# Performance work log

Measured on AMD Instinct MI355X. Metric: run time of the kernel, lower is better.

Reference implementation:

```python
import jax, jax.numpy as jnp
import numpy as np

DEPTH = 11          # tree depth
D = 1024            # input_width
H = 32              # hidden_width (leaf MLP)
O = 1024            # output_width
B = 4096            # flattened token batch
N_LEAVES = 2 ** DEPTH
N_NODES = 2 ** DEPTH - 1


def setup_inputs() -> dict:
    key = jax.random.key(0)
    ks = jax.random.split(key, 7)
    f1 = 1.0 / np.sqrt(D)
    f2 = 1.0 / np.sqrt(H)
    u = lambda k, shape, f: jax.random.uniform(k, shape, jnp.float32, -f, f)
    return {
        "x": jax.random.normal(ks[0], (B, D), jnp.float32),
        "node_weights": u(ks[1], (N_NODES, D), f1),
        "node_biases": u(ks[2], (N_NODES,), f1),   # (n_nodes,1) in torch; flattened
        "w1s": u(ks[3], (N_LEAVES, D, H), f1),
        "b1s": u(ks[4], (N_LEAVES, H), f1),
        "w2s": u(ks[5], (N_LEAVES, H, O), f2),
        "b2s": u(ks[6], (N_LEAVES, O), f2),
    }


def reference(x, node_weights, node_biases, w1s, b1s, w2s, b2s):
    # --- hard tree descent (eval_forward) ---
    nodes = jnp.zeros((x.shape[0],), jnp.int32)
    for i in range(DEPTH):  # fixed small loop over tree depth
        w = node_weights[nodes]                       # [B, D] gathered plane coeffs
        b = node_biases[nodes]                        # [B]
        score = jnp.einsum('bd,bd->b', x, w) + b      # per-sample dot product
        choice = (score >= 0).astype(jnp.int32)
        platform = 2 ** i - 1
        next_platform = 2 ** (i + 1) - 1
        nodes = (nodes - platform) * 2 + choice + next_platform
    leaves = nodes - (2 ** DEPTH - 1)                 # [B] leaf index per sample

    # --- per-sample leaf MLP with gathered weights ---
    h = jax.nn.relu(jnp.einsum('bd,bdh->bh', x, w1s[leaves]) + b1s[leaves])  # [B, H]
    out = jnp.einsum('bh,bho->bo', h, w2s[leaves]) + b2s[leaves]             # [B, O]
    return out
```

## Files before the change

kernel.cpp:

```cpp
#include <hip/hip_runtime.h>

#define DEPTH 11
#define D 1024
#define H 32
#define OW 1024
#define B 4096
#define N_LEAVES 2048
#define N_NODES 2047
#define SMAX 4
#define MAX_ITEMS 3072
#define NBLK 768
#define MAXK 4

typedef float f32x4 __attribute__((ext_vector_type(4)));
typedef __attribute__((address_space(3))) void lds_void;
typedef const __attribute__((address_space(1))) void glb_void;

#define SB __builtin_amdgcn_sched_barrier(0)
#define WAITV(N) do { asm volatile("s_waitcnt vmcnt(" #N ")" ::: "memory"); SB; } while (0)
#define WAITLG0  do { asm volatile("s_waitcnt lgkmcnt(0)" ::: "memory"); SB; } while (0)
#define BARRIER  do { WAITLG0; __builtin_amdgcn_s_barrier(); \
                      asm volatile("" ::: "memory"); SB; } while (0)
#define GLOAD(dst, ptr) \
    asm volatile("global_load_dwordx4 %0, %1, off" : "=&v"(dst) : "v"(ptr) : "memory")

__global__ __launch_bounds__(256) void descent_kernel(
    const float* __restrict__ x, const float* __restrict__ nw,
    const float* __restrict__ nb, int* __restrict__ leaf,
    int* __restrict__ rnk, int* __restrict__ count)
{
    int lane = threadIdx.x & 63;
    int wv   = threadIdx.x >> 6;
    int samp = blockIdx.x * 4 + wv;

    const float4* xp = (const float4*)(x + (size_t)samp * D);
    float4 xf[4];
#pragma unroll
    for (int k = 0; k < 4; k++) xf[k] = xp[lane + 64 * k];

    int node = 0;
#pragma unroll
    for (int i = 0; i < DEPTH; i++) {
        const float4* wp = (const float4*)(nw + (size_t)node * D);
        double s = 0.0;
#pragma unroll
        for (int k = 0; k < 4; k++) {
            float4 wf = wp[lane + 64 * k];
            s += (double)xf[k].x * (double)wf.x;
            s += (double)xf[k].y * (double)wf.y;
            s += (double)xf[k].z * (double)wf.z;
            s += (double)xf[k].w * (double)wf.w;
        }
#pragma unroll
        for (int m = 32; m >= 1; m >>= 1) s += __shfl_xor(s, m, 64);
        double score = s + (double)nb[node];
        int choice = (score >= 0.0) ? 1 : 0;
        node = 2 * node + 1 + choice;
    }
    int lf = node - N_NODES;
    if (lane == 0) {
        leaf[samp] = lf;
        rnk[samp]  = atomicAdd(&count[lf], 1);
    }
}

__global__ __launch_bounds__(256) void scan_kernel(
    const int* __restrict__ count, int* __restrict__ offsets)
{
    __shared__ int tot[256];
    int t = threadIdx.x;
    int c[8], s = 0;
#pragma unroll
    for (int k = 0; k < 8; k++) { c[k] = count[t * 8 + k]; s += c[k]; }
    tot[t] = s;
    __syncthreads();
    for (int off = 1; off < 256; off <<= 1) {
        int v = (t >= off) ? tot[t - off] : 0;
        __syncthreads();
        tot[t] += v;
        __syncthreads();
    }
    int base = (t > 0) ? tot[t - 1] : 0;
#pragma unroll
    for (int k = 0; k < 8; k++) { offsets[t * 8 + k] = base; base += c[k]; }
}

__global__ __launch_bounds__(256) void scatter_kernel(
    const int* __restrict__ leaf, const int* __restrict__ rnk,
    const int* __restrict__ offsets, int* __restrict__ bucket)
{
    int i = blockIdx.x * 256 + threadIdx.x;
    bucket[offsets[leaf[i]] + rnk[i]] = i;
}

__global__ __launch_bounds__(256) void build_items_kernel(
    const int* __restrict__ count, int* __restrict__ items,
    int* __restrict__ nitems)
{
    int l = blockIdx.x * 256 + threadIdx.x;
    int c = count[l];
    if (c > 0) {
        int k = (c + SMAX - 1) / SMAX;
        int base = atomicAdd(nitems, k);
        for (int i = 0; i < k; i++)
            items[base + i] = l | ((i * SMAX) << 11);
    }
}

__global__ __launch_bounds__(256, 3) void mlp_kernel(
    const float* __restrict__ x, const float* __restrict__ w1s,
    const float* __restrict__ b1s, const float* __restrict__ w2s,
    const float* __restrict__ b2s, const int* __restrict__ offsets,
    const int* __restrict__ count, const int* __restrict__ bucket,
    const int* __restrict__ items, const int* __restrict__ nitems,
    float* __restrict__ out)
{
    __shared__ __align__(16) float xs[SMAX][D];
    __shared__ __align__(16) float pl1[4][SMAX][32];
    __shared__ __align__(16) float hs[SMAX][32];
    __shared__ __align__(16) float b1l[2][4][64];
    __shared__ __align__(16) float b2l[2][4][256];
    __shared__ int md_leaf[MAXK];
    __shared__ int md_sid[MAXK][4];

    const int tid = threadIdx.x, lane = tid & 63, wave = tid >> 6;
    const int dg = lane >> 3, lane4 = lane * 4;
    const int bid = blockIdx.x;

    int nit = nitems[0];
    if (tid < MAXK) {
        int idx = bid + tid * NBLK;
        if (idx < nit) {
            int it = items[idx];
            int l = it & (N_LEAVES - 1), st = it >> 11;
            int c = count[l] - st;
            int S = (c < SMAX) ? c : SMAX;
            int off = offsets[l] + st;
            md_leaf[tid] = l;
            for (int s = 0; s < 4; s++)
                md_sid[tid][s] = bucket[off + ((s < S) ? s : (S - 1))];
        }
    }
    __syncthreads();
    if (bid >= nit) return;
    int n_my = (nit - bid + NBLK - 1) / NBLK;
    if (n_my > MAXK) n_my = MAXK;

    f32x4 w1r[2][4];
    f32x4 w2r[16];

#define L1I(base, cc, bb) do { _Pragma("unroll") \
    for (int u = 0; u < 4; u++) \
        GLOAD(w1r[bb][u], (base) + (cc) * 1024 + u * 256 + lane4); } while (0)

#define L1C(cc, bb) do { _Pragma("unroll") \
    for (int u = 0; u < 4; u++) { \
        f32x4 wv_ = w1r[bb][u]; \
        _Pragma("unroll") \
        for (int s = 0; s < 4; s++) \
            acc[s] += xs[s][wave * 256 + (cc) * 32 + u * 8 + dg] * wv_; } } while (0)

    int lc = md_leaf[0];
    const float* w1x = w1s + (size_t)lc * 32768 + wave * 8192;
    {
#pragma unroll
        for (int pp = 0; pp < 4; pp++)
            __builtin_amdgcn_global_load_lds(
                (glb_void*)(x + (size_t)md_sid[0][pp] * D + wave * 256 + lane4),
                (lds_void*)(&xs[pp][wave * 256]), 16, 0, 0);
        __builtin_amdgcn_global_load_lds(
            (glb_void*)(b1s + lc * H + ((lane < 32) ? lane : 31)),
            (lds_void*)(&b1l[0][wave][0]), 4, 0, 0);
        __builtin_amdgcn_global_load_lds(
            (glb_void*)(b2s + (size_t)lc * OW + wave * 256 + lane4),
            (lds_void*)(&b2l[0][wave][0]), 16, 0, 0);
        L1I(w1x, 0, 0); L1I(w1x, 1, 1);
        L1I(w1x, 0, 0); L1I(w1x, 1, 1);
    }

    for (int k = 0; k < n_my; k++) {
        const int p  = k & 1, pn = p ^ 1;
        const int kn = (k + 1 < n_my) ? k + 1 : k;
        const int ln = md_leaf[kn];
        const float* w2x = w2s + (size_t)lc * 32768 + wave * 256;
        const float* w1n = w1s + (size_t)ln * 32768 + wave * 8192;
        int sidc[4];
#pragma unroll
        for (int s = 0; s < 4; s++) sidc[s] = md_sid[k][s];

        f32x4 acc[4] = {};

        WAITV(8); L1C(0, 0); L1I(w1x, 2, 0);
        WAITV(8); L1C(1, 1); L1I(w1x, 3, 1);
        WAITV(4); L1C(2, 0); L1I(w1x, 4, 0);
        WAITV(4); L1C(3, 1); L1I(w1x, 5, 1);
        WAITV(4); L1C(4, 0); L1I(w1x, 6, 0);
        WAITV(4); L1C(5, 1); L1I(w1x, 7, 1);
        WAITV(4); L1C(6, 0);
#pragma unroll
        for (int j = 0; j < 8; j++) GLOAD(w2r[j], w2x + j * 1024 + lane4);
        WAITV(8); L1C(7, 1);
#pragma unroll
        for (int j = 8; j < 16; j++) GLOAD(w2r[j], w2x + j * 1024 + lane4);

#pragma unroll
        for (int m = 8; m <= 32; m <<= 1)
#pragma unroll
            for (int s = 0; s < 4; s++)
#pragma unroll
                for (int e = 0; e < 4; e++)
                    acc[s][e] += __shfl_xor(acc[s][e], m, 64);
        if (dg == 0) {
#pragma unroll
            for (int s = 0; s < 4; s++)
                *(f32x4*)&pl1[wave][s][(lane & 7) * 4] = acc[s];
        }
        BARRIER;
        if (tid < 128) {
            int s2 = tid >> 5, j2 = tid & 31;
            float sum = pl1[0][s2][j2] + pl1[1][s2][j2] + pl1[2][s2][j2] +
                        pl1[3][s2][j2] + b1l[p][tid >> 6][j2];
            hs[s2][j2] = fmaxf(sum, 0.f);
        }
        BARRIER;

        f32x4 o[4] = {};
#pragma unroll
        for (int jj = 0; jj < 32; jj++) {
            if (jj == 31) { WAITV(14); } else { WAITV(15); }
            f32x4 w = w2r[jj & 15];
#pragma unroll
            for (int s = 0; s < 4; s++) o[s] += hs[s][jj] * w;
            if (jj < 16) {
                GLOAD(w2r[jj & 15], w2x + (jj + 16) * 1024 + lane4);
            } else if (jj < 20) {
                const int pp = jj - 16;
                __builtin_amdgcn_global_load_lds(
                    (glb_void*)(x + (size_t)md_sid[kn][pp] * D + wave * 256 + lane4),
                    (lds_void*)(&xs[pp][wave * 256]), 16, 0, 0);
            } else if (jj == 20) {
                __builtin_amdgcn_global_load_lds(
                    (glb_void*)(b1s + ln * H + ((lane < 32) ? lane : 31)),
                    (lds_void*)(&b1l[pn][wave][0]), 4, 0, 0);
            } else if (jj == 21) {
                __builtin_amdgcn_global_load_lds(
                    (glb_void*)(b2s + (size_t)ln * OW + wave * 256 + lane4),
                    (lds_void*)(&b2l[pn][wave][0]), 16, 0, 0);
            } else if (jj < 26) {
                GLOAD(w1r[0][jj - 22], w1n + (jj - 22) * 256 + lane4);
            } else if (jj < 30) {
                GLOAD(w1r[1][jj - 26], w1n + 1024 + (jj - 26) * 256 + lane4);
            }
        }

        f32x4 bv = *(const f32x4*)&b2l[p][wave][lane4];
#pragma unroll
        for (int s = 0; s < 4; s++) {
            f32x4 ov = o[s] + bv;
            *(f32x4*)(out + (size_t)sidc[s] * OW + wave * 256 + lane4) = ov;
        }
        lc = ln;
        w1x = w1n;
    }
#undef L1I
#undef L1C
}

extern "C" void kernel_launch(void* const* d_in, const int* in_sizes, int n_in,
                              void* d_out, int out_size, void* d_ws, size_t ws_size,
                              hipStream_t stream)
{
    const float* x   = (const float*)d_in[0];
    const float* nw  = (const float*)d_in[1];
    const float* nb  = (const float*)d_in[2];
    const float* w1s = (const float*)d_in[3];
    const float* b1s = (const float*)d_in[4];
    const float* w2s = (const float*)d_in[5];
    const float* b2s = (const float*)d_in[6];
    float* out = (float*)d_out;

    int* leaf    = (int*)d_ws;
    int* rnk     = leaf + B;
    int* count   = rnk + B;
    int* offsets = count + N_LEAVES;
    int* bucket  = offsets + N_LEAVES;
    int* items   = bucket + B;
    int* nitems  = items + MAX_ITEMS;

    hipMemsetAsync(count, 0, N_LEAVES * sizeof(int), stream);
    hipMemsetAsync(nitems, 0, sizeof(int), stream);
    descent_kernel<<<B / 4, 256, 0, stream>>>(x, nw, nb, leaf, rnk, count);
    scan_kernel<<<1, 256, 0, stream>>>(count, offsets);
    scatter_kernel<<<B / 256, 256, 0, stream>>>(leaf, rnk, offsets, bucket);
    build_items_kernel<<<N_LEAVES / 256, 256, 0, stream>>>(count, items, nitems);
    mlp_kernel<<<NBLK, 256, 0, stream>>>(x, w1s, b1s, w2s, b2s,
                                         offsets, count, bucket,
                                         items, nitems, out);
}
```

Measured before the change: 128.1 us.

## Fuse item building into scan, drop a barrier, and hand-schedule the layer-2 loop

```diff
diff --git a/kernel.cpp b/kernel.cpp
--- a/kernel.cpp
+++ b/kernel.cpp
@@ -64,11 +64,14 @@
     }
 }
 
-__global__ __launch_bounds__(256) void scan_kernel(
-    const int* __restrict__ count, int* __restrict__ offsets)
+__global__ __launch_bounds__(256) void scanbuild_kernel(
+    const int* __restrict__ count, int* __restrict__ offsets,
+    int* __restrict__ items, int* __restrict__ nitems)
 {
     __shared__ int tot[256];
+    __shared__ int ln;
     int t = threadIdx.x;
+    if (t == 0) ln = 0;
     int c[8], s = 0;
 #pragma unroll
     for (int k = 0; k < 8; k++) { c[k] = count[t * 8 + k]; s += c[k]; }
@@ -81,8 +84,20 @@
         __syncthreads();
     }
     int base = (t > 0) ? tot[t - 1] : 0;
-#pragma unroll
-    for (int k = 0; k < 8; k++) { offsets[t * 8 + k] = base; base += c[k]; }
+    int myit = 0;
+#pragma unroll
+    for (int k = 0; k < 8; k++) myit += (c[k] + SMAX - 1) / SMAX;
+    int ibase = (myit > 0) ? atomicAdd(&ln, myit) : 0;
+#pragma unroll
+    for (int k = 0; k < 8; k++) {
+        offsets[t * 8 + k] = base;
+        int ki = (c[k] + SMAX - 1) / SMAX;
+        for (int i = 0; i < ki; i++)
+            items[ibase++] = (t * 8 + k) | ((i * SMAX) << 11);
+        base += c[k];
+    }
+    __syncthreads();
+    if (t == 0) nitems[0] = ln;
 }
 
 __global__ __launch_bounds__(256) void scatter_kernel(
@@ -91,20 +106,6 @@
 {
     int i = blockIdx.x * 256 + threadIdx.x;
     bucket[offsets[leaf[i]] + rnk[i]] = i;
-}
-
-__global__ __launch_bounds__(256) void build_items_kernel(
-    const int* __restrict__ count, int* __restrict__ items,
-    int* __restrict__ nitems)
-{
-    int l = blockIdx.x * 256 + threadIdx.x;
-    int c = count[l];
-    if (c > 0) {
-        int k = (c + SMAX - 1) / SMAX;
-        int base = atomicAdd(nitems, k);
-        for (int i = 0; i < k; i++)
-            items[base + i] = l | ((i * SMAX) << 11);
-    }
 }
 
 __global__ __launch_bounds__(256, 3) void mlp_kernel(
@@ -116,8 +117,8 @@
     float* __restrict__ out)
 {
     __shared__ __align__(16) float xs[SMAX][D];
-    __shared__ __align__(16) float pl1[4][SMAX][32];
-    __shared__ __align__(16) float hs[SMAX][32];
+    __shared__ __align__(16) float pl1[2][4][SMAX][32];
+    __shared__ __align__(16) float hs_w[4][SMAX][32];
     __shared__ __align__(16) float b1l[2][4][64];
     __shared__ __align__(16) float b2l[2][4][256];
     __shared__ int md_leaf[MAXK];
@@ -160,22 +161,26 @@
         for (int s = 0; s < 4; s++) \
             acc[s] += xs[s][wave * 256 + (cc) * 32 + u * 8 + dg] * wv_; } } while (0)
 
+#define STAGE_X(KK, PP) \
+    __builtin_amdgcn_global_load_lds( \
+        (glb_void*)(x + (size_t)md_sid[KK][PP] * D + wave * 256 + lane4), \
+        (lds_void*)(&xs[PP][wave * 256]), 16, 0, 0)
+#define STAGE_B1(LL, PP) \
+    __builtin_amdgcn_global_load_lds( \
+        (glb_void*)(b1s + (LL) * H + ((lane < 32) ? lane : 31)), \
+        (lds_void*)(&b1l[PP][wave][0]), 4, 0, 0)
+#define STAGE_B2(LL, PP) \
+    __builtin_amdgcn_global_load_lds( \
+        (glb_void*)(b2s + (size_t)(LL) * OW + wave * 256 + lane4), \
+        (lds_void*)(&b2l[PP][wave][0]), 16, 0, 0)
+
     int lc = md_leaf[0];
     const float* w1x = w1s + (size_t)lc * 32768 + wave * 8192;
     {
-#pragma unroll
-        for (int pp = 0; pp < 4; pp++)
-            __builtin_amdgcn_global_load_lds(
-                (glb_void*)(x + (size_t)md_sid[0][pp] * D + wave * 256 + lane4),
-                (lds_void*)(&xs[pp][wave * 256]), 16, 0, 0);
-        __builtin_amdgcn_global_load_lds(
-            (glb_void*)(b1s + lc * H + ((lane < 32) ? lane : 31)),
-            (lds_void*)(&b1l[0][wave][0]), 4, 0, 0);
-        __builtin_amdgcn_global_load_lds(
-            (glb_void*)(b2s + (size_t)lc * OW + wave * 256 + lane4),
-            (lds_void*)(&b2l[0][wave][0]), 16, 0, 0);
+        STAGE_X(0, 0); STAGE_X(0, 1); STAGE_X(0, 2); STAGE_X(0, 3);
+        STAGE_B1(lc, 0); STAGE_B2(lc, 0);
         L1I(w1x, 0, 0); L1I(w1x, 1, 1);
-        L1I(w1x, 0, 0); L1I(w1x, 1, 1);
+        L1I(w1x, 1, 1);
     }
 
     for (int k = 0; k < n_my; k++) {
@@ -190,16 +195,16 @@
 
         f32x4 acc[4] = {};
 
-        WAITV(8); L1C(0, 0); L1I(w1x, 2, 0);
-        WAITV(8); L1C(1, 1); L1I(w1x, 3, 1);
-        WAITV(4); L1C(2, 0); L1I(w1x, 4, 0);
-        WAITV(4); L1C(3, 1); L1I(w1x, 5, 1);
-        WAITV(4); L1C(4, 0); L1I(w1x, 6, 0);
-        WAITV(4); L1C(5, 1); L1I(w1x, 7, 1);
-        WAITV(4); L1C(6, 0);
+        WAITV(8); L1C(0, 0); SB; L1I(w1x, 2, 0);
+        WAITV(8); L1C(1, 1); SB; L1I(w1x, 3, 1);
+        WAITV(4); L1C(2, 0); SB; L1I(w1x, 4, 0);
+        WAITV(4); L1C(3, 1); SB; L1I(w1x, 5, 1);
+        WAITV(4); L1C(4, 0); SB; L1I(w1x, 6, 0);
+        WAITV(4); L1C(5, 1); SB; L1I(w1x, 7, 1);
+        WAITV(4); L1C(6, 0); SB;
 #pragma unroll
         for (int j = 0; j < 8; j++) GLOAD(w2r[j], w2x + j * 1024 + lane4);
-        WAITV(8); L1C(7, 1);
+        WAITV(8); L1C(7, 1); SB;
 #pragma unroll
         for (int j = 8; j < 16; j++) GLOAD(w2r[j], w2x + j * 1024 + lane4);
 
@@ -213,45 +218,63 @@
         if (dg == 0) {
 #pragma unroll
             for (int s = 0; s < 4; s++)
-                *(f32x4*)&pl1[wave][s][(lane & 7) * 4] = acc[s];
+                *(f32x4*)&pl1[p][wave][s][(lane & 7) * 4] = acc[s];
         }
         BARRIER;
-        if (tid < 128) {
-            int s2 = tid >> 5, j2 = tid & 31;
-            float sum = pl1[0][s2][j2] + pl1[1][s2][j2] + pl1[2][s2][j2] +
-                        pl1[3][s2][j2] + b1l[p][tid >> 6][j2];
-            hs[s2][j2] = fmaxf(sum, 0.f);
-        }
-        BARRIER;
-
+
+        {
+            int v = lane * 2, s2 = v >> 5, j2 = v & 31;
+            float ha = pl1[p][0][s2][j2] + pl1[p][1][s2][j2] +
+                       pl1[p][2][s2][j2] + pl1[p][3][s2][j2] + b1l[p][wave][j2];
+            float hb = pl1[p][0][s2][j2 + 1] + pl1[p][1][s2][j2 + 1] +
+                       pl1[p][2][s2][j2 + 1] + pl1[p][3][s2][j2 + 1] +
+                       b1l[p][wave][j2 + 1];
+            float2 hv;
+            hv.x = fmaxf(ha, 0.f);
+            hv.y = fmaxf(hb, 0.f);
+            *(float2*)&hs_w[wave][s2][j2] = hv;
+        }
+        WAITLG0;
+
+        const float(*hw)[32] = hs_w[wave];
         f32x4 o[4] = {};
-#pragma unroll
-        for (int jj = 0; jj < 32; jj++) {
-            if (jj == 31) { WAITV(14); } else { WAITV(15); }
-            f32x4 w = w2r[jj & 15];
-#pragma unroll
-            for (int s = 0; s < 4; s++) o[s] += hs[s][jj] * w;
-            if (jj < 16) {
-                GLOAD(w2r[jj & 15], w2x + (jj + 16) * 1024 + lane4);
-            } else if (jj < 20) {
-                const int pp = jj - 16;
-                __builtin_amdgcn_global_load_lds(
-                    (glb_void*)(x + (size_t)md_sid[kn][pp] * D + wave * 256 + lane4),
-                    (lds_void*)(&xs[pp][wave * 256]), 16, 0, 0);
-            } else if (jj == 20) {
-                __builtin_amdgcn_global_load_lds(
-                    (glb_void*)(b1s + ln * H + ((lane < 32) ? lane : 31)),
-                    (lds_void*)(&b1l[pn][wave][0]), 4, 0, 0);
-            } else if (jj == 21) {
-                __builtin_amdgcn_global_load_lds(
-                    (glb_void*)(b2s + (size_t)ln * OW + wave * 256 + lane4),
-                    (lds_void*)(&b2l[pn][wave][0]), 16, 0, 0);
-            } else if (jj < 26) {
-                GLOAD(w1r[0][jj - 22], w1n + (jj - 22) * 256 + lane4);
-            } else if (jj < 30) {
-                GLOAD(w1r[1][jj - 26], w1n + 1024 + (jj - 26) * 256 + lane4);
-            }
-        }
+
+#define L2CMP(JJ) do { f32x4 w_ = w2r[(JJ) & 15]; _Pragma("unroll") \
+    for (int s = 0; s < 4; s++) o[s] += hw[s][JJ] * w_; } while (0)
+
+        WAITV(15); L2CMP(0);  SB; GLOAD(w2r[0],  w2x + 16 * 1024 + lane4);
+        WAITV(15); L2CMP(1);  SB; GLOAD(w2r[1],  w2x + 17 * 1024 + lane4);
+        WAITV(15); L2CMP(2);  SB; GLOAD(w2r[2],  w2x + 18 * 1024 + lane4);
+        WAITV(15); L2CMP(3);  SB; GLOAD(w2r[3],  w2x + 19 * 1024 + lane4);
+        WAITV(15); L2CMP(4);  SB; GLOAD(w2r[4],  w2x + 20 * 1024 + lane4);
+        WAITV(15); L2CMP(5);  SB; GLOAD(w2r[5],  w2x + 21 * 1024 + lane4);
+        WAITV(15); L2CMP(6);  SB; GLOAD(w2r[6],  w2x + 22 * 1024 + lane4);
+        WAITV(15); L2CMP(7);  SB; GLOAD(w2r[7],  w2x + 23 * 1024 + lane4);
+        WAITV(15); L2CMP(8);  SB; GLOAD(w2r[8],  w2x + 24 * 1024 + lane4);
+        WAITV(15); L2CMP(9);  SB; GLOAD(w2r[9],  w2x + 25 * 1024 + lane4);
+        WAITV(15); L2CMP(10); SB; GLOAD(w2r[10], w2x + 26 * 1024 + lane4);
+        WAITV(15); L2CMP(11); SB; GLOAD(w2r[11], w2x + 27 * 1024 + lane4);
+        WAITV(15); L2CMP(12); SB; GLOAD(w2r[12], w2x + 28 * 1024 + lane4);
+        WAITV(15); L2CMP(13); SB; GLOAD(w2r[13], w2x + 29 * 1024 + lane4);
+        WAITV(15); L2CMP(14); SB; GLOAD(w2r[14], w2x + 30 * 1024 + lane4);
+        WAITV(15); L2CMP(15); SB; GLOAD(w2r[15], w2x + 31 * 1024 + lane4);
+        WAITV(15); L2CMP(16); SB; STAGE_X(kn, 0);
+        WAITV(15); L2CMP(17); SB; STAGE_X(kn, 1);
+        WAITV(15); L2CMP(18); SB; STAGE_X(kn, 2);
+        WAITV(15); L2CMP(19); SB; STAGE_X(kn, 3);
+        WAITV(15); L2CMP(20); SB; STAGE_B1(ln, pn);
+        WAITV(15); L2CMP(21); SB; STAGE_B2(ln, pn);
+        WAITV(15); L2CMP(22); SB; L1I(w1n, 0, 0);
+        WAITV(18); L2CMP(23); SB; L1I(w1n, 1, 1);
+        WAITV(21); L2CMP(24); SB;
+        WAITV(20); L2CMP(25); SB;
+        WAITV(19); L2CMP(26); SB;
+        WAITV(18); L2CMP(27); SB;
+        WAITV(17); L2CMP(28); SB;
+        WAITV(16); L2CMP(29); SB;
+        WAITV(15); L2CMP(30); SB;
+        WAITV(14); L2CMP(31); SB;
+#undef L2CMP
 
         f32x4 bv = *(const f32x4*)&b2l[p][wave][lane4];
 #pragma unroll
@@ -264,6 +287,9 @@
     }
 #undef L1I
 #undef L1C
+#undef STAGE_X
+#undef STAGE_B1
+#undef STAGE_B2
 }
 
 extern "C" void kernel_launch(void* const* d_in, const int* in_sizes, int n_in,
@@ -288,11 +314,9 @@
     int* nitems  = items + MAX_ITEMS;
 
     hipMemsetAsync(count, 0, N_LEAVES * sizeof(int), stream);
-    hipMemsetAsync(nitems, 0, sizeof(int), stream);
     descent_kernel<<<B / 4, 256, 0, stream>>>(x, nw, nb, leaf, rnk, count);
-    scan_kernel<<<1, 256, 0, stream>>>(count, offsets);
+    scanbuild_kernel<<<1, 256, 0, stream>>>(count, offsets, items, nitems);
     scatter_kernel<<<B / 256, 256, 0, stream>>>(leaf, rnk, offsets, bucket);
-    build_items_kernel<<<N_LEAVES / 256, 256, 0, stream>>>(count, items, nitems);
     mlp_kernel<<<NBLK, 256, 0, stream>>>(x, w1s, b1s, w2s, b2s,
                                          offsets, count, bucket,
                                          items, nitems, out);
```

Measured after the change: 125.0 us. -2.4%, faster.
